# Performance work log

Measured on AMD Instinct MI355X. Metric: run time of the kernel, lower is better.

The kernel has to match this reference:

```python
import jax, jax.numpy as jnp
import numpy as np

C_IN = 128
DIM = 2 * C_IN          # ELAN final channels = 2*in_channels = 256
WS = 8                  # window size
HEADS = 8
HEAD_DIM = DIM // HEADS
B, H, W = 4, 128, 128
LN_EPS = 1e-5


def setup_inputs() -> dict:
    key = jax.random.key(0)
    ks = jax.random.split(key, 20)
    mid = C_IN // 2  # middle_channels == block_channels == 64

    def p(k, shape, scale=0.05):
        return jax.random.normal(k, shape, jnp.float32) * scale

    return dict(
        x=jax.random.normal(ks[0], (B, C_IN, H, W), jnp.float32),
        # ELAN stem 1x1 convs: [main, short], each folded BN (scale, bias)
        w_stem=p(ks[1], (2, mid, C_IN, 1, 1)),
        s_stem=1.0 + p(ks[2], (2, mid)),
        b_stem=p(ks[3], (2, mid)),
        # 2 blocks x 2 convs of 3x3, mid->mid
        w_blk=p(ks[4], (4, mid, mid, 3, 3)),
        s_blk=1.0 + p(ks[5], (4, mid)),
        b_blk=p(ks[6], (4, mid)),
        # SwinV2 block params
        norm1_g=jnp.ones((DIM,), jnp.float32),
        norm1_b=jnp.zeros((DIM,), jnp.float32),
        qkv_w=p(ks[7], (3 * DIM, DIM)),
        qkv_b=p(ks[8], (3 * DIM,)).at[DIM:2 * DIM].set(0.0),  # V2 zeroes k bias
        proj_w=p(ks[9], (DIM, DIM)),
        proj_b=p(ks[10], (DIM,)),
        logit_scale=jnp.full((HEADS, 1, 1), float(np.log(10.0)), jnp.float32),
        cpb_w1=p(ks[11], (512, 2)),
        cpb_b1=p(ks[12], (512,)),
        cpb_w2=p(ks[13], (HEADS, 512)),
        norm2_g=jnp.ones((DIM,), jnp.float32),
        norm2_b=jnp.zeros((DIM,), jnp.float32),
        mlp_w1=p(ks[14], (DIM, DIM)),  # mlp_ratio=1.0
        mlp_b1=p(ks[15], (DIM,)),
        mlp_w2=p(ks[16], (DIM, DIM)),
        mlp_b2=p(ks[17], (DIM,)),
    )


def convbn(x, w, s, b, pad):
    # Conv(no bias) + eval-mode BN folded into per-channel scale/bias + SiLU
    y = jax.lax.conv_general_dilated(
        x, w, (1, 1), [(pad, pad), (pad, pad)],
        dimension_numbers=("NCHW", "OIHW", "NCHW"))
    y = y * s[None, :, None, None] + b[None, :, None, None]
    return jax.nn.silu(y)


def layernorm(x, g, b):
    m = jnp.mean(x, -1, keepdims=True)
    v = jnp.var(x, -1, keepdims=True)
    return (x - m) * jax.lax.rsqrt(v + LN_EPS) * g + b


def _rel_bias_consts():
    ws = WS
    ch = np.arange(-(ws - 1), ws, dtype=np.float32)
    table = np.stack(np.meshgrid(ch, ch, indexing="ij"), axis=-1)  # [2ws-1,2ws-1,2]
    table = table / (ws - 1) * 8.0
    table = np.sign(table) * np.log2(np.abs(table) + 1.0) / 3.0
    coords = np.stack(np.meshgrid(np.arange(ws), np.arange(ws), indexing="ij")).reshape(2, -1)
    rel = (coords[:, :, None] - coords[:, None, :]).transpose(1, 2, 0)  # [N,N,2]
    rel[..., 0] += ws - 1
    rel[..., 1] += ws - 1
    rel[..., 0] *= 2 * ws - 1
    idx = rel.sum(-1).reshape(-1)
    return jnp.asarray(table.reshape(-1, 2)), jnp.asarray(idx)


_TABLE, _IDX = _rel_bias_consts()


def elan_swin(x, w_stem, s_stem, b_stem, w_blk, s_blk, b_blk, norm1_g, norm1_b,
              qkv_w, qkv_b, proj_w, proj_b, logit_scale, cpb_w1, cpb_b1, cpb_w2,
              norm2_g, norm2_b, mlp_w1, mlp_b1, mlp_w2, mlp_b2):
    # ---- ELANBlock ----
    x_short = convbn(x, w_stem[1], s_stem[1], b_stem[1], 0)
    x_main = convbn(x, w_stem[0], s_stem[0], b_stem[0], 0)
    xb = x_main
    outs = []
    for i in range(2):
        xb = convbn(xb, w_blk[2 * i], s_blk[2 * i], b_blk[2 * i], 1)
        xb = convbn(xb, w_blk[2 * i + 1], s_blk[2 * i + 1], b_blk[2 * i + 1], 1)
        outs.append(xb)
    e = jnp.concatenate([outs[1], outs[0], x_main, x_short], axis=1)  # [B,DIM,H,W]
    e = e.transpose(0, 2, 3, 1)  # NHWC

    # ---- ShiftedWindowAttentionV2 (shift=0, H,W divisible by WS) ----
    Bn, Hh, Ww, Cc = e.shape
    nH, nW = Hh // WS, Ww // WS
    N = WS * WS
    xw = e.reshape(Bn, nH, WS, nW, WS, Cc).transpose(0, 1, 3, 2, 4, 5).reshape(-1, N, Cc)
    qkv = xw @ qkv_w.T + qkv_b
    qkv = qkv.reshape(-1, N, 3, HEADS, HEAD_DIM).transpose(2, 0, 3, 1, 4)
    q, k, v = qkv[0], qkv[1], qkv[2]  # [Bw, heads, N, d]
    qn = q / jnp.maximum(jnp.linalg.norm(q, axis=-1, keepdims=True), 1e-12)
    kn = k / jnp.maximum(jnp.linalg.norm(k, axis=-1, keepdims=True), 1e-12)
    attn = jnp.einsum("whnd,whmd->whnm", qn, kn)
    scale = jnp.exp(jnp.minimum(logit_scale, jnp.log(100.0)))  # [heads,1,1]
    attn = attn * scale[None]
    # continuous position bias MLP
    bias = jax.nn.relu(_TABLE @ cpb_w1.T + cpb_b1) @ cpb_w2.T  # [(2ws-1)^2, heads]
    bias = bias[_IDX].reshape(N, N, HEADS).transpose(2, 0, 1)
    bias = 16.0 * jax.nn.sigmoid(bias)
    attn = jax.nn.softmax(attn + bias[None], axis=-1)
    out = jnp.einsum("whnm,whmd->whnd", attn, v).transpose(0, 2, 1, 3).reshape(-1, N, Cc)
    out = out @ proj_w.T + proj_b
    out = out.reshape(Bn, nH, nW, WS, WS, Cc).transpose(0, 1, 3, 2, 4, 5).reshape(Bn, Hh, Ww, Cc)

    # ---- SwinTransformerBlockV2 (post-norm residuals) ----
    s = e + layernorm(out, norm1_g, norm1_b)
    h = s @ mlp_w1.T + mlp_b1
    h = jax.nn.gelu(h, approximate=False)
    h = h @ mlp_w2.T + mlp_b2
    s = s + layernorm(h, norm2_g, norm2_b)
    return s.transpose(0, 3, 1, 2)  # NCHW


def reference(x, w_stem, s_stem, b_stem, w_blk, s_blk, b_blk, norm1_g, norm1_b,
              qkv_w, qkv_b, proj_w, proj_b, logit_scale, cpb_w1, cpb_b1, cpb_w2,
              norm2_g, norm2_b, mlp_w1, mlp_b1, mlp_w2, mlp_b2):
    return elan_swin(x, w_stem, s_stem, b_stem, w_blk, s_blk, b_blk, norm1_g, norm1_b,
                     qkv_w, qkv_b, proj_w, proj_b, logit_scale, cpb_w1, cpb_b1, cpb_w2,
                     norm2_g, norm2_b, mlp_w1, mlp_b1, mlp_w2, mlp_b2)
```

## Files before the change

kernel.cpp:

```cpp
#include <hip/hip_runtime.h>
#include <hip/hip_bf16.h>
#include <math.h>


#define HW 16384
typedef unsigned int u32;
typedef unsigned short u16;
typedef __attribute__((ext_vector_type(8))) short short8;
typedef __attribute__((ext_vector_type(4))) float floatx4;

#define MEMBAR() asm volatile("" ::: "memory")

__device__ __forceinline__ float silu_f(float y) { return y / (1.f + expf(-y)); }
__device__ __forceinline__ float bflo(u32 u) { return __uint_as_float(u << 16); }
__device__ __forceinline__ float bfhi(u32 u) { return __uint_as_float(u & 0xffff0000u); }
__device__ __forceinline__ float bf2f(u16 v) { return __uint_as_float((u32)v << 16); }
__device__ __forceinline__ u16 f2bf(float x) {
  u32 u = __float_as_uint(x);
  u += 0x7fffu + ((u >> 16) & 1u);
  return (u16)(u >> 16);
}
__device__ __forceinline__ u32 pack2(float a, float b) {
  return (u32)f2bf(a) | ((u32)f2bf(b) << 16);
}
__device__ __forceinline__ short8 mk8(u32 a, u32 b, u32 c, u32 d) {
  union { u32 u[4]; short8 s; } t;
  t.u[0] = a; t.u[1] = b; t.u[2] = c; t.u[3] = d;
  return t.s;
}
__device__ __forceinline__ u32 shfl_sel(u32 va, u32 vb, int s, bool sel) {
  u32 x = (u32)__shfl((int)va, s);
  u32 y = (u32)__shfl((int)vb, s);
  return sel ? y : x;
}

#define GLDS16(gp, lp)                                           \
  __builtin_amdgcn_global_load_lds(                              \
      (const __attribute__((address_space(1))) void*)(gp),       \
      (__attribute__((address_space(3))) void*)(lp), 16, 0, 0)

__global__ __launch_bounds__(256) void prep_kernel(
    const float* __restrict__ w_blk, const float* __restrict__ s_blk,
    const float* __restrict__ w_stem, const float* __restrict__ s_stem,
    const float* __restrict__ qkv_w, const float* __restrict__ proj_w,
    const float* __restrict__ mlp_w1, const float* __restrict__ mlp_w2,
    u16* __restrict__ wtc, u16* __restrict__ wts, u16* __restrict__ qwb,
    u16* __restrict__ pwb, u16* __restrict__ m1wb, u16* __restrict__ m2wb) {
  int idx = blockIdx.x * 256 + threadIdx.x;
  if (idx < 147456) {
    int c = idx & 63;
    int rest = idx >> 6;
    int oc = rest & 63;
    int ct = rest >> 6;
    int conv = ct / 9, t = ct % 9;
    float w = w_blk[((size_t)(conv * 64 + oc) * 64 + c) * 9 + t];
    wtc[idx] = f2bf(w * s_blk[conv * 64 + oc]);
  } else if (idx < 163840) {
    int j = idx - 147456;
    int c = j & 127, oc = j >> 7;
    wts[j] = f2bf(w_stem[(size_t)oc * 128 + c] * s_stem[oc]);
  } else if (idx < 360448) {
    int j = idx - 163840;
    qwb[j] = f2bf(qkv_w[j]);
  } else if (idx < 425984) {
    int j = idx - 360448;
    pwb[j] = f2bf(proj_w[j]);
  } else if (idx < 491520) {
    int j = idx - 425984;
    m1wb[j] = f2bf(mlp_w1[j]);
  } else if (idx < 557056) {
    int j = idx - 491520;
    m2wb[j] = f2bf(mlp_w2[j]);
  }
}

__global__ __launch_bounds__(512) void cpb_mlp_kernel(
    const float* __restrict__ w1, const float* __restrict__ b1,
    const float* __restrict__ w2, float* __restrict__ pre) {
  __shared__ float hb[512];
  int t = blockIdx.x, j = threadIdx.x;
  int i = t / 15, jj = t % 15;
  float c0 = (float)(i - 7) * (8.f / 7.f);
  float c1 = (float)(jj - 7) * (8.f / 7.f);
  float s0 = (c0 > 0.f) ? 1.f : ((c0 < 0.f) ? -1.f : 0.f);
  float s1 = (c1 > 0.f) ? 1.f : ((c1 < 0.f) ? -1.f : 0.f);
  float t0 = s0 * log2f(fabsf(c0) + 1.f) * (1.f / 3.f);
  float t1 = s1 * log2f(fabsf(c1) + 1.f) * (1.f / 3.f);
  float h = t0 * w1[j * 2] + t1 * w1[j * 2 + 1] + b1[j];
  hb[j] = fmaxf(h, 0.f);
  __syncthreads();
  if (j < 8) {
    float s = 0.f;
    for (int k = 0; k < 512; ++k) s += hb[k] * w2[j * 512 + k];
    pre[t * 8 + j] = s;
  }
}

__global__ __launch_bounds__(256) void cpb_expand_kernel(
    const float* __restrict__ pre, float* __restrict__ bias_t) {
  int idx = blockIdx.x * 256 + threadIdx.x;
  int m = idx >> 6, n = idx & 63;
  int di = (n >> 3) - (m >> 3) + 7;
  int dj = (n & 7) - (m & 7) + 7;
  int ti = di * 15 + dj;
#pragma unroll
  for (int h = 0; h < 8; ++h) {
    float v = pre[ti * 8 + h];
    bias_t[h * 4096 + idx] = 16.f / (1.f + expf(-v));
  }
}

__global__ __launch_bounds__(256) void transpose_in_kernel(
    const float* __restrict__ x, u16* __restrict__ xt) {
  __shared__ float tl[64][65];
  int bid = blockIdx.x;
  int b = bid >> 9;
  int r = bid & 511;
  int cs = r >> 8, hws = r & 255;
  int c0 = cs << 6, hw0 = hws << 6;
  int tid = threadIdx.x;
  for (int e = tid; e < 4096; e += 256) {
    int c = e >> 6, p = e & 63;
    tl[c][p] = x[(size_t)(b * 128 + c0 + c) * HW + hw0 + p];
  }
  __syncthreads();
  for (int e = tid; e < 4096; e += 256) {
    int p = e >> 6, c = e & 63;
    xt[(size_t)(b * HW + hw0 + p) * 128 + c0 + c] = f2bf(tl[c][p]);
  }
}

__global__ __launch_bounds__(256, 4) void gemm_bf16_kernel(
    const u16* __restrict__ A, const u16* __restrict__ W,
    const float* __restrict__ bias, u16* __restrict__ C, int K, int ldc,
    int act) {
  __shared__ u16 As[128 * 64];
  __shared__ u16 Ws[64 * 64];
  int tid = threadIdx.x;
  int wv = tid >> 6, lane = tid & 63;
  int m0 = blockIdx.y * 128, n0 = blockIdx.x * 64;
  floatx4 zz = {0.f, 0.f, 0.f, 0.f};
  floatx4 acc[2][4];
#pragma unroll
  for (int i = 0; i < 2; ++i)
#pragma unroll
    for (int j = 0; j < 4; ++j) acc[i][j] = zz;
  int lr = lane >> 3, ls = lane & 7;
  for (int k0 = 0; k0 < K; k0 += 64) {
#pragma unroll
    for (int i = 0; i < 4; ++i) {
      int ci = wv * 4 + i;
      int r = ci * 8 + lr;
      int cc = ls ^ (r & 7);
      GLDS16(A + (size_t)(m0 + r) * K + k0 + cc * 8, As + ci * 512);
    }
#pragma unroll
    for (int i = 0; i < 2; ++i) {
      int ci = wv * 2 + i;
      int r = ci * 8 + lr;
      int cc = ls ^ (r & 7);
      GLDS16(W + (size_t)(n0 + r) * K + k0 + cc * 8, Ws + ci * 512);
    }
    __syncthreads();
#pragma unroll
    for (int kk = 0; kk < 2; ++kk) {
      int g = kk * 4 + (lane >> 4);
      short8 a0, a1, b0, b1, b2, b3;
      {
        int row = wv * 32 + (lane & 15);
        a0 = *(const short8*)&As[row * 64 + (g ^ (row & 7)) * 8];
        int row2 = row + 16;
        a1 = *(const short8*)&As[row2 * 64 + (g ^ (row2 & 7)) * 8];
      }
      {
        int col = lane & 15;
        b0 = *(const short8*)&Ws[col * 64 + (g ^ (col & 7)) * 8];
        int c1 = col + 16;
        b1 = *(const short8*)&Ws[c1 * 64 + (g ^ (c1 & 7)) * 8];
        int c2 = col + 32;
        b2 = *(const short8*)&Ws[c2 * 64 + (g ^ (c2 & 7)) * 8];
        int c3 = col + 48;
        b3 = *(const short8*)&Ws[c3 * 64 + (g ^ (c3 & 7)) * 8];
      }
      acc[0][0] = __builtin_amdgcn_mfma_f32_16x16x32_bf16(a0, b0, acc[0][0], 0, 0, 0);
      acc[0][1] = __builtin_amdgcn_mfma_f32_16x16x32_bf16(a0, b1, acc[0][1], 0, 0, 0);
      acc[0][2] = __builtin_amdgcn_mfma_f32_16x16x32_bf16(a0, b2, acc[0][2], 0, 0, 0);
      acc[0][3] = __builtin_amdgcn_mfma_f32_16x16x32_bf16(a0, b3, acc[0][3], 0, 0, 0);
      acc[1][0] = __builtin_amdgcn_mfma_f32_16x16x32_bf16(a1, b0, acc[1][0], 0, 0, 0);
      acc[1][1] = __builtin_amdgcn_mfma_f32_16x16x32_bf16(a1, b1, acc[1][1], 0, 0, 0);
      acc[1][2] = __builtin_amdgcn_mfma_f32_16x16x32_bf16(a1, b2, acc[1][2], 0, 0, 0);
      acc[1][3] = __builtin_amdgcn_mfma_f32_16x16x32_bf16(a1, b3, acc[1][3], 0, 0, 0);
    }
    __syncthreads();
  }
  int rbase = wv * 32 + ((lane >> 4) << 2);
  int cb = lane & 15;
#pragma unroll
  for (int mi = 0; mi < 2; ++mi) {
#pragma unroll
    for (int nj = 0; nj < 4; ++nj) {
      int col = n0 + nj * 16 + cb;
      float bv = bias[col];
#pragma unroll
      for (int r = 0; r < 4; ++r) {
        int row = m0 + rbase + mi * 16 + r;
        float v = acc[mi][nj][r] + bv;
        if (act == 1) v = 0.5f * v * (1.f + erff(v * 0.70710678118654752f));
        else if (act == 2) v = silu_f(v);
        C[(size_t)row * ldc + col] = f2bf(v);
      }
    }
  }
}

__global__ __launch_bounds__(256) void conv3x3_mfma_kernel(
    const u16* __restrict__ in, int istr, u16* __restrict__ outp, int ostr,
    const u16* __restrict__ wt, const float* __restrict__ bias) {
  __shared__ u16 tile[6400];
  int tid = threadIdx.x;
  int wv = tid >> 6, lane = tid & 63;
  int bx = blockIdx.x, by = blockIdx.y, b = blockIdx.z;
  int h0 = by * 8, w0 = bx * 8;
#pragma unroll
  for (int rr = 0; rr < 4; ++rr) {
    int slot = rr * 256 + tid;
    int p = slot >> 3, ch = slot & 7;
    if (p < 100) {
      int hr = p / 10, hc = p % 10;
      int gh = h0 + hr - 1, gw = w0 + hc - 1;
      bool ok = (gh >= 0) && (gh < 128) && (gw >= 0) && (gw < 128);
      uint4 v = {0u, 0u, 0u, 0u};
      if (ok) {
        size_t pix = (size_t)((b * 128 + gh) * 128 + gw);
        v = *(const uint4*)(in + pix * istr + ch * 8);
      }
      *(uint4*)(tile + p * 64 + ((ch ^ (p & 7)) << 3)) = v;
    }
  }
  __syncthreads();
  int pl = lane & 15;
  int g = lane >> 4;
  int prow = 2 * wv + (pl >> 3), pcol = pl & 7;
  floatx4 zz = {0.f, 0.f, 0.f, 0.f};
  floatx4 acc[4] = {zz, zz, zz, zz};
#pragma unroll
  for (int t = 0; t < 9; ++t) {
    int dy = t / 3, dx = t % 3;
    int hp = (prow + dy) * 10 + (pcol + dx);
    short8 bf0 = *(const short8*)&tile[hp * 64 + (((0 * 4 + g) ^ (hp & 7)) << 3)];
    short8 bf1 = *(const short8*)&tile[hp * 64 + (((1 * 4 + g) ^ (hp & 7)) << 3)];
    const u16* wtap = wt + t * 4096;
#pragma unroll
    for (int nf = 0; nf < 4; ++nf) {
      short8 a0 = *(const short8*)&wtap[(nf * 16 + pl) * 64 + g * 8];
      short8 a1 = *(const short8*)&wtap[(nf * 16 + pl) * 64 + 32 + g * 8];
      acc[nf] = __builtin_amdgcn_mfma_f32_16x16x32_bf16(a0, bf0, acc[nf], 0, 0, 0);
      acc[nf] = __builtin_amdgcn_mfma_f32_16x16x32_bf16(a1, bf1, acc[nf], 0, 0, 0);
    }
  }
  size_t pix = (size_t)((b * 128 + h0 + prow) * 128 + w0 + pcol);
#pragma unroll
  for (int nf = 0; nf < 4; ++nf) {
    float o0 = silu_f(acc[nf][0] + bias[nf * 16 + g * 4 + 0]);
    float o1 = silu_f(acc[nf][1] + bias[nf * 16 + g * 4 + 1]);
    float o2 = silu_f(acc[nf][2] + bias[nf * 16 + g * 4 + 2]);
    float o3 = silu_f(acc[nf][3] + bias[nf * 16 + g * 4 + 3]);
    uint2 w2;
    w2.x = pack2(o0, o1);
    w2.y = pack2(o2, o3);
    *(uint2*)(outp + pix * ostr + nf * 16 + g * 4) = w2;
  }
}

__device__ __forceinline__ void qkv_mm(const u16* Elds, const u16* qwb,
                                       int moff, int h, int lc, int lg,
                                       floatx4 acc[4][2]) {
  floatx4 zz = {0.f, 0.f, 0.f, 0.f};
#pragma unroll
  for (int mf = 0; mf < 4; ++mf) {
    acc[mf][0] = zz;
    acc[mf][1] = zz;
  }
#pragma unroll
  for (int ks = 0; ks < 8; ++ks) {
    int ch = ks >> 1, g = ((ks & 1) << 2) + lg;
    short8 af[4];
#pragma unroll
    for (int mf = 0; mf < 4; ++mf) {
      int tk = mf * 16 + lc;
      af[mf] = *(const short8*)&Elds[(ch * 64 + tk) * 64 + ((g ^ (tk & 7)) << 3)];
    }
#pragma unroll
    for (int nf = 0; nf < 2; ++nf) {
      short8 bf = *(const short8*)(qwb +
          (size_t)(moff + h * 32 + nf * 16 + lc) * 256 + ks * 32 + lg * 8);
#pragma unroll
      for (int mf = 0; mf < 4; ++mf)
        acc[mf][nf] =
            __builtin_amdgcn_mfma_f32_16x16x32_bf16(af[mf], bf, acc[mf][nf], 0, 0, 0);
    }
  }
}

__global__ __launch_bounds__(512, 4) void attn_fused_kernel(
    const u16* __restrict__ ebf, const u16* __restrict__ qwb,
    const float* __restrict__ qkv_b, const float* __restrict__ logit_scale,
    const float* __restrict__ bias_t, u16* __restrict__ ao) {
  __shared__ __align__(16) char lds[73728];
  int tid = threadIdx.x;
  int w = tid >> 6, l = tid & 63;
  int wid = blockIdx.x;
  int h = __builtin_amdgcn_readfirstlane(w);
  u16* Elds = (u16*)lds;
  char* Sc = lds + 32768 + w * 5120;
  char* Ol = Sc;

  int b = wid >> 8, wh = (wid >> 4) & 15, ww = wid & 15;
  int pixbase = (b << 14) + wh * 1024 + ww * 8;
  {
    int lr = l >> 3, ls = l & 7;
    int ch = w >> 1;
#pragma unroll
    for (int j = 0; j < 4; ++j) {
      int jj = ((w & 1) << 2) + j;
      int pix = pixbase + jj * 128 + lr;
      GLDS16(ebf + (size_t)pix * 256 + ch * 64 + ((ls ^ lr) << 3),
             Elds + (ch * 8 + jj) * 512);
    }
  }
  __syncthreads();

  int lc = l & 15, lg = l >> 4;
  float scale = __expf(fminf(logit_scale[h], 4.6051701860f));
  floatx4 macc[4][2];
  short8 kf[4], qf[4];

  qkv_mm(Elds, qwb, 256, h, lc, lg, macc);
#pragma unroll
  for (int mf = 0; mf < 4; ++mf)
#pragma unroll
    for (int r = 0; r < 4; ++r) {
      float v0 = macc[mf][0][r], v1 = macc[mf][1][r];
      float ss = v0 * v0 + v1 * v1;
      ss += __shfl_xor(ss, 1);
      ss += __shfl_xor(ss, 2);
      ss += __shfl_xor(ss, 4);
      ss += __shfl_xor(ss, 8);
      float rk = 1.f / fmaxf(sqrtf(ss), 1e-12f);
      int tk = mf * 16 + (lg << 2) + r;
      *(u16*)(Sc + tk * 80 + lc * 2) = f2bf(v0 * rk);
      *(u16*)(Sc + tk * 80 + (16 + lc) * 2) = f2bf(v1 * rk);
    }
  MEMBAR();
#pragma unroll
  for (int i = 0; i < 4; ++i)
    kf[i] = *(const short8*)(Sc + (i * 16 + lc) * 80 + (lg << 4));
  MEMBAR();

  qkv_mm(Elds, qwb, 0, h, lc, lg, macc);
  {
    float qb0 = qkv_b[h * 32 + lc], qb1 = qkv_b[h * 32 + 16 + lc];
#pragma unroll
    for (int mf = 0; mf < 4; ++mf)
#pragma unroll
      for (int r = 0; r < 4; ++r) {
        float v0 = macc[mf][0][r] + qb0, v1 = macc[mf][1][r] + qb1;
        float ss = v0 * v0 + v1 * v1;
        ss += __shfl_xor(ss, 1);
        ss += __shfl_xor(ss, 2);
        ss += __shfl_xor(ss, 4);
        ss += __shfl_xor(ss, 8);
        float rq = scale / fmaxf(sqrtf(ss), 1e-12f);
        int tk = mf * 16 + (lg << 2) + r;
        *(u16*)(Sc + tk * 80 + lc * 2) = f2bf(v0 * rq);
        *(u16*)(Sc + tk * 80 + (16 + lc) * 2) = f2bf(v1 * rq);
      }
    MEMBAR();
#pragma unroll
    for (int i = 0; i < 4; ++i)
      qf[i] = *(const short8*)(Sc + (i * 16 + lc) * 80 + (lg << 4));
    MEMBAR();
  }

  u32 v01[4][2], v23[4][2];
  qkv_mm(Elds, qwb, 512, h, lc, lg, macc);
  {
    float vb0 = qkv_b[512 + h * 32 + lc], vb1 = qkv_b[512 + h * 32 + 16 + lc];
#pragma unroll
    for (int mf = 0; mf < 4; ++mf) {
      v01[mf][0] = pack2(macc[mf][0][0] + vb0, macc[mf][0][1] + vb0);
      v23[mf][0] = pack2(macc[mf][0][2] + vb0, macc[mf][0][3] + vb0);
      v01[mf][1] = pack2(macc[mf][1][0] + vb1, macc[mf][1][1] + vb1);
      v23[mf][1] = pack2(macc[mf][1][2] + vb1, macc[mf][1][3] + vb1);
    }
  }

  floatx4 zz = {0.f, 0.f, 0.f, 0.f};
  floatx4 S[4][4];
#pragma unroll
  for (int mi = 0; mi < 4; ++mi)
#pragma unroll
    for (int ni = 0; ni < 4; ++ni)
      S[mi][ni] = __builtin_amdgcn_mfma_f32_16x16x32_bf16(kf[mi], qf[ni], zz, 0, 0, 0);

  const float* bh = bias_t + h * 4096;
  float den[4] = {0.f, 0.f, 0.f, 0.f};
#pragma unroll
  for (int mi = 0; mi < 4; ++mi) {
    int mb = mi * 16 + (lg << 2);
#pragma unroll
    for (int ni = 0; ni < 4; ++ni) {
      int nn = ni * 16 + lc;
#pragma unroll
      for (int r = 0; r < 4; ++r) {
        float e = __expf(S[mi][ni][r] + bh[(mb + r) * 64 + nn]);
        S[mi][ni][r] = e;
        den[ni] += e;
      }
    }
  }
#pragma unroll
  for (int ni = 0; ni < 4; ++ni) {
    den[ni] += __shfl_xor(den[ni], 16);
    den[ni] += __shfl_xor(den[ni], 32);
    den[ni] = 1.f / den[ni];
  }
  u32 p01[4][4], p23[4][4];
#pragma unroll
  for (int mi = 0; mi < 4; ++mi)
#pragma unroll
    for (int ni = 0; ni < 4; ++ni) {
      p01[mi][ni] = pack2(S[mi][ni][0] * den[ni], S[mi][ni][1] * den[ni]);
      p23[mi][ni] = pack2(S[mi][ni][2] * den[ni], S[mi][ni][3] * den[ni]);
    }

  int s1 = ((lg & 1) << 5) + lc;
  int s2 = s1 + 16;
  bool hi = lg >= 2;
  short8 vf[2][2];
#pragma unroll
  for (int ks = 0; ks < 2; ++ks)
#pragma unroll
    for (int db = 0; db < 2; ++db) {
      u32 w0 = shfl_sel(v01[ks * 2][db], v01[ks * 2 + 1][db], s1, hi);
      u32 w1 = shfl_sel(v23[ks * 2][db], v23[ks * 2 + 1][db], s1, hi);
      u32 w2 = shfl_sel(v01[ks * 2][db], v01[ks * 2 + 1][db], s2, hi);
      u32 w3 = shfl_sel(v23[ks * 2][db], v23[ks * 2 + 1][db], s2, hi);
      vf[ks][db] = mk8(w0, w1, w2, w3);
    }
  floatx4 O[4][2];
#pragma unroll
  for (int nb = 0; nb < 4; ++nb) {
    u32 a0 = shfl_sel(p01[0][nb], p01[1][nb], s1, hi);
    u32 a1 = shfl_sel(p23[0][nb], p23[1][nb], s1, hi);
    u32 a2 = shfl_sel(p01[0][nb], p01[1][nb], s2, hi);
    u32 a3 = shfl_sel(p23[0][nb], p23[1][nb], s2, hi);
    short8 pf0 = mk8(a0, a1, a2, a3);
    u32 b0 = shfl_sel(p01[2][nb], p01[3][nb], s1, hi);
    u32 b1 = shfl_sel(p23[2][nb], p23[3][nb], s1, hi);
    u32 b2 = shfl_sel(p01[2][nb], p01[3][nb], s2, hi);
    u32 b3 = shfl_sel(p23[2][nb], p23[3][nb], s2, hi);
    short8 pf1 = mk8(b0, b1, b2, b3);
    floatx4 o0 = __builtin_amdgcn_mfma_f32_16x16x32_bf16(pf0, vf[0][0], zz, 0, 0, 0);
    o0 = __builtin_amdgcn_mfma_f32_16x16x32_bf16(pf1, vf[1][0], o0, 0, 0, 0);
    floatx4 o1 = __builtin_amdgcn_mfma_f32_16x16x32_bf16(pf0, vf[0][1], zz, 0, 0, 0);
    o1 = __builtin_amdgcn_mfma_f32_16x16x32_bf16(pf1, vf[1][1], o1, 0, 0, 0);
    O[nb][0] = o0;
    O[nb][1] = o1;
  }

#pragma unroll
  for (int nb = 0; nb < 4; ++nb)
#pragma unroll
    for (int r = 0; r < 4; ++r) {
      int n = nb * 16 + (lg << 2) + r;
      *(u16*)(Ol + n * 72 + lc * 2) = f2bf(O[nb][0][r]);
      *(u16*)(Ol + n * 72 + (16 + lc) * 2) = f2bf(O[nb][1][r]);
    }
  MEMBAR();
  u32 ov[16];
#pragma unroll
  for (int j = 0; j < 16; ++j) ov[j] = *(const u32*)(Ol + l * 72 + j * 4);
  uint4* op = (uint4*)(ao + (size_t)(wid * 64 + l) * 256 + h * 32);
#pragma unroll
  for (int q4 = 0; q4 < 4; ++q4) {
    uint4 v;
    v.x = ov[q4 * 4 + 0];
    v.y = ov[q4 * 4 + 1];
    v.z = ov[q4 * 4 + 2];
    v.w = ov[q4 * 4 + 3];
    op[q4] = v;
  }
}

__global__ __launch_bounds__(256) void ln1v_kernel(
    const u16* __restrict__ pin, const u16* __restrict__ ebf,
    u16* __restrict__ sbf, const float* __restrict__ g,
    const float* __restrict__ bb) {
  int tid = threadIdx.x;
  int bid = blockIdx.x;
  int b = bid >> 8, hw0 = (bid & 255) << 6;
  int i = tid >> 2, qq = tid & 3;
  int hw = hw0 + i;
  int him = hw >> 7, wim = hw & 127;
  int wid = b * 256 + (him >> 3) * 16 + (wim >> 3);
  int t = wid * 64 + (him & 7) * 8 + (wim & 7);
  size_t pbase = (size_t)t * 256 + qq * 64;
  size_t ebase = ((size_t)(b * HW + hw)) * 256 + qq * 64;
  float v[64];
  float s1 = 0.f, s2 = 0.f;
#pragma unroll
  for (int j = 0; j < 8; ++j) {
    uint4 u = *(const uint4*)(pin + pbase + j * 8);
    u32 ua[4] = {u.x, u.y, u.z, u.w};
#pragma unroll
    for (int k = 0; k < 4; ++k) {
      float a = bflo(ua[k]), c = bfhi(ua[k]);
      v[j * 8 + 2 * k] = a;
      v[j * 8 + 2 * k + 1] = c;
      s1 += a + c;
      s2 += a * a + c * c;
    }
  }
  s1 += __shfl_xor(s1, 1);
  s1 += __shfl_xor(s1, 2);
  s2 += __shfl_xor(s2, 1);
  s2 += __shfl_xor(s2, 2);
  float mean = s1 * (1.f / 256.f);
  float var = s2 * (1.f / 256.f) - mean * mean;
  float rs = rsqrtf(var + 1e-5f);
#pragma unroll
  for (int j = 0; j < 8; ++j) {
    uint4 u = *(const uint4*)(ebf + ebase + j * 8);
    u32 ua[4] = {u.x, u.y, u.z, u.w};
    uint4 o;
    u32 ow[4];
#pragma unroll
    for (int k = 0; k < 4; ++k) {
      int c = qq * 64 + j * 8 + 2 * k;
      float o0 = bflo(ua[k]) + (v[j * 8 + 2 * k] - mean) * rs * g[c] + bb[c];
      float o1 = bfhi(ua[k]) + (v[j * 8 + 2 * k + 1] - mean) * rs * g[c + 1] + bb[c + 1];
      ow[k] = pack2(o0, o1);
    }
    o.x = ow[0]; o.y = ow[1]; o.z = ow[2]; o.w = ow[3];
    *(uint4*)(sbf + ebase + j * 8) = o;
  }
}

__global__ __launch_bounds__(256, 4) void gemm_ln2_kernel(
    const u16* __restrict__ A, const u16* __restrict__ W,
    const float* __restrict__ bias, const float* __restrict__ g,
    const float* __restrict__ bb, const u16* __restrict__ res,
    float* __restrict__ outf) {
  __shared__ __align__(16) char lds[40960];
  u16* As = (u16*)lds;
  u16* Ws = (u16*)(lds + 8192);
  u16* Ct = (u16*)lds;
  int tid = threadIdx.x;
  int w = tid >> 6, l = tid & 63;
  int lr = l >> 3, ls = l & 7;
  int lc = l & 15, lg = l >> 4;
  int m0 = blockIdx.x << 6;
  floatx4 zz = {0.f, 0.f, 0.f, 0.f};
  floatx4 acc[16];
#pragma unroll
  for (int i = 0; i < 16; ++i) acc[i] = zz;
  for (int k0 = 0; k0 < 256; k0 += 64) {
#pragma unroll
    for (int j = 0; j < 2; ++j) {
      int ci = w * 2 + j;
      int r = ci * 8 + lr;
      GLDS16(A + (size_t)(m0 + r) * 256 + k0 + ((ls ^ (r & 7)) << 3),
             As + ci * 512);
    }
#pragma unroll
    for (int j = 0; j < 8; ++j) {
      int ci = w * 8 + j;
      int r = ci * 8 + lr;
      GLDS16(W + (size_t)r * 256 + k0 + ((ls ^ (r & 7)) << 3), Ws + ci * 512);
    }
    __syncthreads();
#pragma unroll
    for (int kk = 0; kk < 2; ++kk) {
      int gg = (kk << 2) + lg;
      int arow = w * 16 + lc;
      short8 af = *(const short8*)&As[arow * 64 + ((gg ^ (arow & 7)) << 3)];
#pragma unroll
      for (int nf = 0; nf < 16; ++nf) {
        int crow = nf * 16 + lc;
        short8 bf = *(const short8*)&Ws[crow * 64 + ((gg ^ (crow & 7)) << 3)];
        acc[nf] = __builtin_amdgcn_mfma_f32_16x16x32_bf16(af, bf, acc[nf], 0, 0, 0);
      }
    }
    __syncthreads();
  }
#pragma unroll
  for (int nf = 0; nf < 16; ++nf) {
    float bv = bias[nf * 16 + lc];
#pragma unroll
    for (int r = 0; r < 4; ++r)
      Ct[(w * 16 + (lg << 2) + r) * 264 + nf * 16 + lc] = f2bf(acc[nf][r] + bv);
  }
  __syncthreads();
  int i = tid >> 2, qq = tid & 3;
  float s1 = 0.f, s2 = 0.f;
#pragma unroll
  for (int j2 = 0; j2 < 8; ++j2) {
    uint4 u = *(const uint4*)&Ct[i * 264 + qq * 64 + j2 * 8];
    u32 ua[4] = {u.x, u.y, u.z, u.w};
#pragma unroll
    for (int k = 0; k < 4; ++k) {
      float a = bflo(ua[k]), c = bfhi(ua[k]);
      s1 += a + c;
      s2 += a * a + c * c;
    }
  }
  s1 += __shfl_xor(s1, 1);
  s1 += __shfl_xor(s1, 2);
  s2 += __shfl_xor(s2, 1);
  s2 += __shfl_xor(s2, 2);
  float mean = s1 * (1.f / 256.f);
  float var = s2 * (1.f / 256.f) - mean * mean;
  float rs = rsqrtf(var + 1e-5f);
  int p = m0 + i;
  int b = p >> 14, hw = p & 16383;
  size_t rbase = (size_t)p * 256 + qq * 64;
#pragma unroll
  for (int j2 = 0; j2 < 8; ++j2) {
    uint4 cu = *(const uint4*)&Ct[i * 264 + qq * 64 + j2 * 8];
    u32 ca[4] = {cu.x, cu.y, cu.z, cu.w};
    uint4 u = *(const uint4*)(res + rbase + j2 * 8);
    u32 ua[4] = {u.x, u.y, u.z, u.w};
#pragma unroll
    for (int k = 0; k < 4; ++k) {
      int c = qq * 64 + j2 * 8 + 2 * k;
      float o0 = bflo(ua[k]) + (bflo(ca[k]) - mean) * rs * g[c] + bb[c];
      float o1 = bfhi(ua[k]) + (bfhi(ca[k]) - mean) * rs * g[c + 1] + bb[c + 1];
      outf[(size_t)(b * 256 + c) * HW + hw] = o0;
      outf[(size_t)(b * 256 + c + 1) * HW + hw] = o1;
    }
  }
}

extern "C" void kernel_launch(void* const* d_in, const int* in_sizes, int n_in,
                              void* d_out, int out_size, void* d_ws, size_t ws_size,
                              hipStream_t stream) {
  const float* x        = (const float*)d_in[0];
  const float* w_stem   = (const float*)d_in[1];
  const float* s_stem   = (const float*)d_in[2];
  const float* b_stem   = (const float*)d_in[3];
  const float* w_blk    = (const float*)d_in[4];
  const float* s_blk    = (const float*)d_in[5];
  const float* b_blk    = (const float*)d_in[6];
  const float* norm1_g  = (const float*)d_in[7];
  const float* norm1_b  = (const float*)d_in[8];
  const float* qkv_w    = (const float*)d_in[9];
  const float* qkv_b    = (const float*)d_in[10];
  const float* proj_w   = (const float*)d_in[11];
  const float* proj_b   = (const float*)d_in[12];
  const float* logit_sc = (const float*)d_in[13];
  const float* cpb_w1   = (const float*)d_in[14];
  const float* cpb_b1   = (const float*)d_in[15];
  const float* cpb_w2   = (const float*)d_in[16];
  const float* norm2_g  = (const float*)d_in[17];
  const float* norm2_b  = (const float*)d_in[18];
  const float* mlp_w1   = (const float*)d_in[19];
  const float* mlp_b1   = (const float*)d_in[20];
  const float* mlp_w2   = (const float*)d_in[21];
  const float* mlp_b2   = (const float*)d_in[22];
  float* out = (float*)d_out;
  float* ws = (float*)d_ws;
  (void)in_sizes; (void)n_in; (void)out_size; (void)ws_size;

  float* R0 = ws;
  float* R1 = ws + 16777216;
  float* R2 = ws + 33554432;
  float* TAIL = ws + 50331648;
  u16* WTC  = (u16*)TAIL;
  u16* WTS  = (u16*)(TAIL + 73728);
  u16* QWB  = (u16*)(TAIL + 81920);
  u16* PWB  = (u16*)(TAIL + 180224);
  u16* M1WB = (u16*)(TAIL + 212992);
  u16* M2WB = (u16*)(TAIL + 245760);
  float* BPRE = TAIL + 278528;
  float* BFT  = TAIL + 280576;

  u16* XT  = (u16*)R2;
  u16* EBF = (u16*)(R2 + 8388608);
  u16* T1  = (u16*)R1;
  u16* T2  = (u16*)(R1 + 2097152);
  u16* AO  = (u16*)R0;
  u16* P   = (u16*)(R0 + 8388608);
  u16* SBF = (u16*)R0;
  u16* Hb  = (u16*)R2;

  prep_kernel<<<2176, 256, 0, stream>>>(w_blk, s_blk, w_stem, s_stem, qkv_w,
                                        proj_w, mlp_w1, mlp_w2, WTC, WTS, QWB,
                                        PWB, M1WB, M2WB);
  cpb_mlp_kernel<<<225, 512, 0, stream>>>(cpb_w1, cpb_b1, cpb_w2, BPRE);
  cpb_expand_kernel<<<16, 256, 0, stream>>>(BPRE, BFT);

  transpose_in_kernel<<<2048, 256, 0, stream>>>(x, XT);
  dim3 gs(2, 512);
  gemm_bf16_kernel<<<gs, 256, 0, stream>>>(XT, WTS, b_stem, EBF + 128, 128, 256, 2);

  dim3 cgrid(16, 16, 4);
  conv3x3_mfma_kernel<<<cgrid, 256, 0, stream>>>(EBF + 128, 256, T1, 64, WTC, b_blk);
  conv3x3_mfma_kernel<<<cgrid, 256, 0, stream>>>(T1, 64, EBF + 64, 256, WTC + 9 * 4096, b_blk + 64);
  conv3x3_mfma_kernel<<<cgrid, 256, 0, stream>>>(EBF + 64, 256, T2, 64, WTC + 18 * 4096, b_blk + 128);
  conv3x3_mfma_kernel<<<cgrid, 256, 0, stream>>>(T2, 64, EBF, 256, WTC + 27 * 4096, b_blk + 192);

  attn_fused_kernel<<<1024, 512, 0, stream>>>(EBF, QWB, qkv_b, logit_sc, BFT, AO);

  dim3 g4(4, 512);
  gemm_bf16_kernel<<<g4, 256, 0, stream>>>(AO, PWB, proj_b, P, 256, 256, 0);
  ln1v_kernel<<<1024, 256, 0, stream>>>(P, EBF, SBF, norm1_g, norm1_b);
  gemm_bf16_kernel<<<g4, 256, 0, stream>>>(SBF, M1WB, mlp_b1, Hb, 256, 256, 1);
  gemm_ln2_kernel<<<1024, 256, 0, stream>>>(Hb, M2WB, mlp_b2, norm2_g, norm2_b,
                                            SBF, out);
}
```

Before: 410.1 us.

## Shrink attention LDS footprint and pair-interleave bias table for vector loads

Cuts the attention kernel's shared memory from 72KB to 52KB. It stages the normalized K and Q fragments in two halves of 32 rows each, and reuses the E tile region (after a barrier) for the output transpose. Launch bounds are raised to allow 6 waves per SIMD. The relative-position bias table is re-laid out so adjacent row pairs are interleaved, which lets the softmax read float2 values. The extra barrier and halved staging add some serialization, and the higher occupancy target may limit registers.

```diff
diff --git a/kernel.cpp b/kernel.cpp
--- a/kernel.cpp
+++ b/kernel.cpp
@@ -106,7 +106,8 @@
 #pragma unroll
   for (int h = 0; h < 8; ++h) {
     float v = pre[ti * 8 + h];
-    bias_t[h * 4096 + idx] = 16.f / (1.f + expf(-v));
+    bias_t[h * 4096 + (((m >> 1) * 64 + n) << 1) + (m & 1)] =
+        16.f / (1.f + expf(-v));
   }
 }
 
@@ -302,18 +303,17 @@
   }
 }
 
-__global__ __launch_bounds__(512, 4) void attn_fused_kernel(
+__global__ __launch_bounds__(512, 6) void attn_fused_kernel(
     const u16* __restrict__ ebf, const u16* __restrict__ qwb,
     const float* __restrict__ qkv_b, const float* __restrict__ logit_scale,
     const float* __restrict__ bias_t, u16* __restrict__ ao) {
-  __shared__ __align__(16) char lds[73728];
+  __shared__ __align__(16) char lds[53248];
   int tid = threadIdx.x;
   int w = tid >> 6, l = tid & 63;
   int wid = blockIdx.x;
   int h = __builtin_amdgcn_readfirstlane(w);
   u16* Elds = (u16*)lds;
-  char* Sc = lds + 32768 + w * 5120;
-  char* Ol = Sc;
+  char* Sc = lds + 32768 + w * 2560;
 
   int b = wid >> 8, wh = (wid >> 4) & 15, ww = wid & 15;
   int pixbase = (b << 14) + wh * 1024 + ww * 8;
@@ -337,49 +337,59 @@
 
   qkv_mm(Elds, qwb, 256, h, lc, lg, macc);
 #pragma unroll
-  for (int mf = 0; mf < 4; ++mf)
-#pragma unroll
-    for (int r = 0; r < 4; ++r) {
-      float v0 = macc[mf][0][r], v1 = macc[mf][1][r];
-      float ss = v0 * v0 + v1 * v1;
-      ss += __shfl_xor(ss, 1);
-      ss += __shfl_xor(ss, 2);
-      ss += __shfl_xor(ss, 4);
-      ss += __shfl_xor(ss, 8);
-      float rk = 1.f / fmaxf(sqrtf(ss), 1e-12f);
-      int tk = mf * 16 + (lg << 2) + r;
-      *(u16*)(Sc + tk * 80 + lc * 2) = f2bf(v0 * rk);
-      *(u16*)(Sc + tk * 80 + (16 + lc) * 2) = f2bf(v1 * rk);
-    }
-  MEMBAR();
-#pragma unroll
-  for (int i = 0; i < 4; ++i)
-    kf[i] = *(const short8*)(Sc + (i * 16 + lc) * 80 + (lg << 4));
-  MEMBAR();
-
-  qkv_mm(Elds, qwb, 0, h, lc, lg, macc);
-  {
-    float qb0 = qkv_b[h * 32 + lc], qb1 = qkv_b[h * 32 + 16 + lc];
-#pragma unroll
-    for (int mf = 0; mf < 4; ++mf)
+  for (int half = 0; half < 2; ++half) {
+#pragma unroll
+    for (int mf2 = 0; mf2 < 2; ++mf2) {
+      int mf = half * 2 + mf2;
 #pragma unroll
       for (int r = 0; r < 4; ++r) {
-        float v0 = macc[mf][0][r] + qb0, v1 = macc[mf][1][r] + qb1;
+        float v0 = macc[mf][0][r], v1 = macc[mf][1][r];
         float ss = v0 * v0 + v1 * v1;
         ss += __shfl_xor(ss, 1);
         ss += __shfl_xor(ss, 2);
         ss += __shfl_xor(ss, 4);
         ss += __shfl_xor(ss, 8);
-        float rq = scale / fmaxf(sqrtf(ss), 1e-12f);
-        int tk = mf * 16 + (lg << 2) + r;
-        *(u16*)(Sc + tk * 80 + lc * 2) = f2bf(v0 * rq);
-        *(u16*)(Sc + tk * 80 + (16 + lc) * 2) = f2bf(v1 * rq);
+        float rk = 1.f / fmaxf(sqrtf(ss), 1e-12f);
+        int tk = mf2 * 16 + (lg << 2) + r;
+        *(u16*)(Sc + tk * 80 + lc * 2) = f2bf(v0 * rk);
+        *(u16*)(Sc + tk * 80 + (16 + lc) * 2) = f2bf(v1 * rk);
       }
+    }
     MEMBAR();
 #pragma unroll
-    for (int i = 0; i < 4; ++i)
-      qf[i] = *(const short8*)(Sc + (i * 16 + lc) * 80 + (lg << 4));
+    for (int i = 0; i < 2; ++i)
+      kf[half * 2 + i] = *(const short8*)(Sc + (i * 16 + lc) * 80 + (lg << 4));
     MEMBAR();
+  }
+
+  qkv_mm(Elds, qwb, 0, h, lc, lg, macc);
+  {
+    float qb0 = qkv_b[h * 32 + lc], qb1 = qkv_b[h * 32 + 16 + lc];
+#pragma unroll
+    for (int half = 0; half < 2; ++half) {
+#pragma unroll
+      for (int mf2 = 0; mf2 < 2; ++mf2) {
+        int mf = half * 2 + mf2;
+#pragma unroll
+        for (int r = 0; r < 4; ++r) {
+          float v0 = macc[mf][0][r] + qb0, v1 = macc[mf][1][r] + qb1;
+          float ss = v0 * v0 + v1 * v1;
+          ss += __shfl_xor(ss, 1);
+          ss += __shfl_xor(ss, 2);
+          ss += __shfl_xor(ss, 4);
+          ss += __shfl_xor(ss, 8);
+          float rq = scale / fmaxf(sqrtf(ss), 1e-12f);
+          int tk = mf2 * 16 + (lg << 2) + r;
+          *(u16*)(Sc + tk * 80 + lc * 2) = f2bf(v0 * rq);
+          *(u16*)(Sc + tk * 80 + (16 + lc) * 2) = f2bf(v1 * rq);
+        }
+      }
+      MEMBAR();
+#pragma unroll
+      for (int i = 0; i < 2; ++i)
+        qf[half * 2 + i] = *(const short8*)(Sc + (i * 16 + lc) * 80 + (lg << 4));
+      MEMBAR();
+    }
   }
 
   u32 v01[4][2], v23[4][2];
@@ -407,15 +417,18 @@
   float den[4] = {0.f, 0.f, 0.f, 0.f};
 #pragma unroll
   for (int mi = 0; mi < 4; ++mi) {
-    int mb = mi * 16 + (lg << 2);
-#pragma unroll
-    for (int ni = 0; ni < 4; ++ni) {
-      int nn = ni * 16 + lc;
-#pragma unroll
-      for (int r = 0; r < 4; ++r) {
-        float e = __expf(S[mi][ni][r] + bh[(mb + r) * 64 + nn]);
-        S[mi][ni][r] = e;
-        den[ni] += e;
+#pragma unroll
+    for (int r2 = 0; r2 < 2; ++r2) {
+      int m2 = mi * 8 + (lg << 1) + r2;
+#pragma unroll
+      for (int ni = 0; ni < 4; ++ni) {
+        int nn = ni * 16 + lc;
+        float2 bp = *(const float2*)(bh + ((m2 * 64 + nn) << 1));
+        float e0 = __expf(S[mi][ni][2 * r2] + bp.x);
+        float e1 = __expf(S[mi][ni][2 * r2 + 1] + bp.y);
+        S[mi][ni][2 * r2] = e0;
+        S[mi][ni][2 * r2 + 1] = e1;
+        den[ni] += e0 + e1;
       }
     }
   }
@@ -469,18 +482,20 @@
     O[nb][1] = o1;
   }
 
+  __syncthreads();
+  char* Ol = lds + (w << 12);
 #pragma unroll
   for (int nb = 0; nb < 4; ++nb)
 #pragma unroll
     for (int r = 0; r < 4; ++r) {
       int n = nb * 16 + (lg << 2) + r;
-      *(u16*)(Ol + n * 72 + lc * 2) = f2bf(O[nb][0][r]);
-      *(u16*)(Ol + n * 72 + (16 + lc) * 2) = f2bf(O[nb][1][r]);
+      *(u16*)(Ol + n * 64 + lc * 2) = f2bf(O[nb][0][r]);
+      *(u16*)(Ol + n * 64 + (16 + lc) * 2) = f2bf(O[nb][1][r]);
     }
   MEMBAR();
   u32 ov[16];
 #pragma unroll
-  for (int j = 0; j < 16; ++j) ov[j] = *(const u32*)(Ol + l * 72 + j * 4);
+  for (int j = 0; j < 16; ++j) ov[j] = *(const u32*)(Ol + l * 64 + j * 4);
   uint4* op = (uint4*)(ao + (size_t)(wid * 64 + l) * 256 + h * 32);
 #pragma unroll
   for (int q4 = 0; q4 < 4; ++q4) {
```

Result: slower. 491.5 us (+19.9%).
